# Kernel tuning notes

Measured on AMD Instinct MI355X. Metric: run time of the kernel, lower is better.

## Reference

```python
import jax, jax.numpy as jnp
import numpy as np

T, A = 2048, 64          # n_thread, n_agents
RAWOB, N_TP, N_GP = 120, 5, 2
E = N_TP * N_GP          # number of sub-nets (type x group placeholder)
D = RAWOB + N_TP + 1     # augmented obs dim fed to each Net
H = 128                  # hidden width of each sub-net MLP
N_ACTION = 16


def setup_inputs() -> dict:
    key = jax.random.key(0)
    ks = jax.random.split(key, 12)
    s1 = 1.0 / np.sqrt(D)
    s2 = 1.0 / np.sqrt(H)
    return {
        "obs": jax.random.normal(ks[0], (T, A, RAWOB), dtype=jnp.float32),
        "hete_pick": jax.random.randint(ks[1], (T, A), 0, E),
        "hete_type": jax.random.randint(ks[2], (T, A), 0, N_TP),
        "gp_sel_summary": jax.random.randint(ks[3], (T, N_TP), 0, N_GP),
        # per-expert actor MLP params [E, ...]
        "W1": jax.random.normal(ks[4], (E, D, H), dtype=jnp.float32) * s1,
        "b1": jnp.zeros((E, H), dtype=jnp.float32),
        "W2": jax.random.normal(ks[5], (E, H, N_ACTION), dtype=jnp.float32) * s2,
        "b2": jnp.zeros((E, N_ACTION), dtype=jnp.float32),
        # central critic params
        "Wc1": jax.random.normal(ks[6], (D, H), dtype=jnp.float32) * s1,
        "bc1": jnp.zeros((H,), dtype=jnp.float32),
        "Wc2": jax.random.normal(ks[7], (H, 1), dtype=jnp.float32) * s2,
        "bc2": jnp.zeros((1,), dtype=jnp.float32),
    }


def _augment_obs(obs, hete_type, gp_sel_summary):
    # obs <- cat(obs, hete_type, gp_sel_summary with -1 scattered at own type idx)
    t, a, _ = obs.shape
    n_tp = gp_sel_summary.shape[1]
    gp = jnp.broadcast_to(gp_sel_summary[:, None, :].astype(obs.dtype), (t, a, n_tp))
    oh = jax.nn.one_hot(hete_type, n_tp, dtype=obs.dtype)
    gp_obs = gp * (1.0 - oh) - oh  # scatter -1 at index hete_type
    return jnp.concatenate([obs, hete_type[..., None].astype(obs.dtype), gp_obs], axis=-1)


def reference(obs, hete_pick, hete_type, gp_sel_summary,
              W1, b1, W2, b2, Wc1, bc1, Wc2, bc2):
    t, a, _ = obs.shape
    x = _augment_obs(obs, hete_type, gp_sel_summary)          # [T, A, D]
    xf = x.reshape(t * a, -1)                                  # [N, D]
    pick = hete_pick.reshape(t * a)                            # [N]
    n_exp = W1.shape[0]
    # dispatch: each token routed to exactly one sub-net; dense compute + masked combine
    logits = jnp.zeros((t * a, W2.shape[-1]), dtype=obs.dtype)
    for e in range(n_exp):  # small fixed expert loop
        y = jax.nn.relu(xf @ W1[e] + b1[e]) @ W2[e] + b2[e]    # [N, n_action]
        logits = jnp.where((pick == e)[:, None], y, logits)
    logits = logits.reshape(t, a, -1)
    # central critic on all tokens
    value = (jax.nn.relu(xf @ Wc1 + bc1) @ Wc2 + bc2).reshape(t, a, 1)
    return logits, value
```

## Files before the change

kernel.cpp:

```cpp
#include <hip/hip_runtime.h>
#include <hip/hip_bf16.h>

#define T_DIM   2048
#define A_DIM   64
#define N_TOK   (T_DIM * A_DIM)
#define RAWOB   120
#define N_TP    5
#define E_EXP   10
#define D_DIM   126
#define DP      128
#define H_DIM   128
#define N_ACT   16
#define CAP     14336
#define MTILE   32
#define MAXC    (CAP / MTILE)
#define LOGITS_SZ (N_TOK * N_ACT)
#define XS_STRIDE 136

typedef __bf16 bh8 __attribute__((ext_vector_type(8)));
typedef float  f32x4 __attribute__((ext_vector_type(4)));

__device__ __forceinline__ f32x4 mfma16(bh8 a, bh8 b, f32x4 c) {
    return __builtin_amdgcn_mfma_f32_16x16x32_bf16(a, b, c, 0, 0, 0);
}

__device__ __forceinline__ ushort f2bf(float f) {
    unsigned x = __builtin_bit_cast(unsigned, f);
    unsigned r = (x + 0x7fffu + ((x >> 16) & 1u)) >> 16;
    return (ushort)r;
}

#define W1T_N (E_EXP * H_DIM * DP)
#define W2T_N (E_EXP * N_ACT * H_DIM)
#define WC1T_N (DP * DP)
#define PREP_BLOCKS 124

__global__ __launch_bounds__(256) void prep_kernel(
    const float* __restrict__ W1, const float* __restrict__ W2,
    const float* __restrict__ Wc1,
    int* __restrict__ counts, ushort* __restrict__ W1t,
    ushort* __restrict__ W2t, ushort* __restrict__ Wc1t)
{
    int bx = blockIdx.x, tid = threadIdx.x;
    if (bx < 44) {
        __shared__ ushort st[32][130];
        const float* src;
        ushort* dstbase;
        int d0;
        if (bx < 40) {
            int e = bx >> 2;
            d0 = (bx & 3) * 32;
            src = W1 + (e * D_DIM + d0) * H_DIM;
            dstbase = W1t + e * H_DIM * DP;
        } else {
            d0 = (bx - 40) * 32;
            src = Wc1 + d0 * H_DIM;
            dstbase = Wc1t;
        }
        int dmax = D_DIM - d0;
#pragma unroll
        for (int p = 0; p < 16; ++p) {
            int idx = p * 256 + tid;
            int dd = idx >> 7, h = idx & 127;
            float v = (dd < dmax) ? src[dd * H_DIM + h] : 0.f;
            st[dd][h] = f2bf(v);
        }
        __syncthreads();
#pragma unroll
        for (int p = 0; p < 16; ++p) {
            int idx = p * 256 + tid;
            int h = idx >> 5, d = idx & 31;
            dstbase[h * DP + d0 + d] = st[d][h];
        }
    } else {
        int i = (bx - 44) * 256 + tid;
        int h = i & 127;
        int a = (i >> 7) & 15;
        int e = i >> 11;
        W2t[(e * N_ACT + a) * H_DIM + h] = f2bf(W2[(e * H_DIM + h) * N_ACT + a]);
        if (bx == 44 && tid < 160) counts[tid] = 0;
    }
}

#define BUCKET_BLOCKS 128
__global__ __launch_bounds__(256) void bucket_kernel(
    const int* __restrict__ pick, int* __restrict__ counts, int* __restrict__ order)
{
    __shared__ int lc[E_EXP], lb[E_EXP], lcur[E_EXP];
    int tid = threadIdx.x;
    if (tid < E_EXP) { lc[tid] = 0; lcur[tid] = 0; }
    __syncthreads();
    int base = blockIdx.x * 1024;
    int e4[4];
#pragma unroll
    for (int it = 0; it < 4; ++it) {
        e4[it] = pick[base + it * 256 + tid];
        atomicAdd(&lc[e4[it]], 1);
    }
    __syncthreads();
    if (tid < E_EXP) lb[tid] = atomicAdd(&counts[tid * 16], lc[tid]);
    __syncthreads();
#pragma unroll
    for (int it = 0; it < 4; ++it) {
        int e = e4[it];
        int pos = lb[e] + atomicAdd(&lcur[e], 1);
        if (pos < CAP) order[e * CAP + pos] = base + it * 256 + tid;
    }
}

__global__ __launch_bounds__(256, 8) void moe_kernel(
    const float* __restrict__ obs, const int* __restrict__ hete_type,
    const int* __restrict__ gp_sel,
    const float* __restrict__ b1, const float* __restrict__ b2,
    const float* __restrict__ bc1, const float* __restrict__ bc2,
    const int* __restrict__ counts, const int* __restrict__ order,
    const ushort* __restrict__ W1t, const ushort* __restrict__ W2t,
    const ushort* __restrict__ Wc1t, const float* __restrict__ Wc2,
    float* __restrict__ out)
{
    __shared__ int idx_s[MTILE];
    __shared__ __align__(16) ushort xs[MTILE * XS_STRIDE];
    __shared__ __align__(16) ushort hs[MTILE * XS_STRIDE];
    __shared__ float red[4][MTILE];

    const int bx = blockIdx.x;
    const int e = bx % E_EXP;
    const int c = bx / E_EXP;
    const int cnt = counts[e * 16];
    const int start = c * MTILE;
    if (start >= cnt) return;
    const int v = min(MTILE, cnt - start);

    const int tid = threadIdx.x;
    if (tid < MTILE) {
        int tok = 0;
        if (tid < v) tok = order[e * CAP + start + tid];
        idx_s[tid] = tok;
    }
    __syncthreads();

    const int ck = (tid & 15) * 8;
    const int r0 = tid >> 4;
#pragma unroll
    for (int j = 0; j < 2; ++j) {
        int row = r0 + j * 16;
        int tok = idx_s[row];
        ushort* dst = &xs[row * XS_STRIDE + ck];
        if (ck < RAWOB) {
            const float* src = obs + tok * RAWOB + ck;
            float4 u0 = *(const float4*)(const void*)src;
            float4 u1 = *(const float4*)(const void*)(src + 4);
            dst[0] = f2bf(u0.x); dst[1] = f2bf(u0.y);
            dst[2] = f2bf(u0.z); dst[3] = f2bf(u0.w);
            dst[4] = f2bf(u1.x); dst[5] = f2bf(u1.y);
            dst[6] = f2bf(u1.z); dst[7] = f2bf(u1.w);
        } else {
            int ht = hete_type[tok];
            int tt = tok >> 6;
            dst[0] = f2bf((float)ht);
#pragma unroll
            for (int q = 0; q < N_TP; ++q) {
                float g = (q == ht) ? -1.0f : (float)gp_sel[tt * N_TP + q];
                dst[1 + q] = f2bf(g);
            }
            dst[6] = 0; dst[7] = 0;
        }
    }
    __syncthreads();

    const int w = tid >> 6;
    const int l = tid & 63;
    const int lm = l & 15;
    const int lq = l >> 4;
    const int n0 = w * 32;

    {
        const ushort* Wt = W1t + e * DP * DP;
        f32x4 acc[2][2];
#pragma unroll
        for (int mt = 0; mt < 2; ++mt) {
            acc[mt][0] = (f32x4){0.f, 0.f, 0.f, 0.f};
            acc[mt][1] = (f32x4){0.f, 0.f, 0.f, 0.f};
        }
#pragma unroll
        for (int kt = 0; kt < 4; ++kt) {
            bh8 bf0 = *(const bh8*)(const void*)(Wt + (n0 + lm) * DP + kt * 32 + lq * 8);
            bh8 bf1 = *(const bh8*)(const void*)(Wt + (n0 + 16 + lm) * DP + kt * 32 + lq * 8);
#pragma unroll
            for (int mt = 0; mt < 2; ++mt) {
                bh8 a = *(const bh8*)(const void*)
                    (xs + (mt * 16 + lm) * XS_STRIDE + kt * 32 + lq * 8);
                acc[mt][0] = mfma16(a, bf0, acc[mt][0]);
                acc[mt][1] = mfma16(a, bf1, acc[mt][1]);
            }
        }
        float bn0 = b1[e * H_DIM + n0 + lm];
        float bn1 = b1[e * H_DIM + n0 + 16 + lm];
#pragma unroll
        for (int mt = 0; mt < 2; ++mt)
#pragma unroll
            for (int nt = 0; nt < 2; ++nt) {
                float bn = nt ? bn1 : bn0;
                int n = n0 + nt * 16 + lm;
#pragma unroll
                for (int r = 0; r < 4; ++r) {
                    int m = mt * 16 + lq * 4 + r;
                    float vf = fmaxf(acc[mt][nt][r] + bn, 0.f);
                    hs[m * XS_STRIDE + n] = f2bf(vf);
                }
            }
    }
    __syncthreads();

    if (w < 2) {
        f32x4 acc2 = (f32x4){0.f, 0.f, 0.f, 0.f};
#pragma unroll
        for (int kt = 0; kt < 4; ++kt) {
            bh8 bf = *(const bh8*)(const void*)
                (W2t + (e * N_ACT + lm) * H_DIM + kt * 32 + lq * 8);
            bh8 a = *(const bh8*)(const void*)
                (hs + (w * 16 + lm) * XS_STRIDE + kt * 32 + lq * 8);
            acc2 = mfma16(a, bf, acc2);
        }
        float bb = b2[e * N_ACT + lm];
#pragma unroll
        for (int r = 0; r < 4; ++r) {
            int m = w * 16 + lq * 4 + r;
            if (m < v) {
                int tok = idx_s[m];
                out[tok * N_ACT + lm] = acc2[r] + bb;
            }
        }
    }

    {
        f32x4 acc[2][2];
#pragma unroll
        for (int mt = 0; mt < 2; ++mt) {
            acc[mt][0] = (f32x4){0.f, 0.f, 0.f, 0.f};
            acc[mt][1] = (f32x4){0.f, 0.f, 0.f, 0.f};
        }
#pragma unroll
        for (int kt = 0; kt < 4; ++kt) {
            bh8 bf0 = *(const bh8*)(const void*)(Wc1t + (n0 + lm) * DP + kt * 32 + lq * 8);
            bh8 bf1 = *(const bh8*)(const void*)(Wc1t + (n0 + 16 + lm) * DP + kt * 32 + lq * 8);
#pragma unroll
            for (int mt = 0; mt < 2; ++mt) {
                bh8 a = *(const bh8*)(const void*)
                    (xs + (mt * 16 + lm) * XS_STRIDE + kt * 32 + lq * 8);
                acc[mt][0] = mfma16(a, bf0, acc[mt][0]);
                acc[mt][1] = mfma16(a, bf1, acc[mt][1]);
            }
        }
        float bn0 = bc1[n0 + lm],   wcv0 = Wc2[n0 + lm];
        float bn1 = bc1[n0 + 16 + lm], wcv1 = Wc2[n0 + 16 + lm];
        float part[2][4];
#pragma unroll
        for (int mt = 0; mt < 2; ++mt)
#pragma unroll
            for (int r = 0; r < 4; ++r)
                part[mt][r] = fmaxf(acc[mt][0][r] + bn0, 0.f) * wcv0
                            + fmaxf(acc[mt][1][r] + bn1, 0.f) * wcv1;
#pragma unroll
        for (int mask = 1; mask < 16; mask <<= 1)
#pragma unroll
            for (int mt = 0; mt < 2; ++mt)
#pragma unroll
                for (int r = 0; r < 4; ++r)
                    part[mt][r] += __shfl_xor(part[mt][r], mask, 64);
        if (lm == 0) {
#pragma unroll
            for (int mt = 0; mt < 2; ++mt)
#pragma unroll
                for (int r = 0; r < 4; ++r)
                    red[w][mt * 16 + lq * 4 + r] = part[mt][r];
        }
    }
    __syncthreads();

    if (tid < MTILE && tid < v) {
        float vt = red[0][tid] + red[1][tid] + red[2][tid] + red[3][tid] + bc2[0];
        out[LOGITS_SZ + idx_s[tid]] = vt;
    }
}

extern "C" void kernel_launch(void* const* d_in, const int* in_sizes, int n_in,
                              void* d_out, int out_size, void* d_ws, size_t ws_size,
                              hipStream_t stream) {
    const float* obs  = (const float*)d_in[0];
    const int*   pick = (const int*)d_in[1];
    const int*   htyp = (const int*)d_in[2];
    const int*   gp   = (const int*)d_in[3];
    const float* W1   = (const float*)d_in[4];
    const float* b1   = (const float*)d_in[5];
    const float* W2   = (const float*)d_in[6];
    const float* b2   = (const float*)d_in[7];
    const float* Wc1  = (const float*)d_in[8];
    const float* bc1  = (const float*)d_in[9];
    const float* Wc2  = (const float*)d_in[10];
    const float* bc2  = (const float*)d_in[11];
    float* out = (float*)d_out;

    int*    counts = (int*)d_ws;
    int*    order  = counts + 160;
    ushort* W1t    = (ushort*)(order + E_EXP * CAP);
    ushort* W2t    = W1t + W1T_N;
    ushort* Wc1t   = W2t + W2T_N;

    prep_kernel<<<PREP_BLOCKS, 256, 0, stream>>>(
        W1, W2, Wc1, counts, W1t, W2t, Wc1t);
    bucket_kernel<<<BUCKET_BLOCKS, 256, 0, stream>>>(pick, counts, order);
    moe_kernel<<<E_EXP * MAXC, 256, 0, stream>>>(
        obs, htyp, gp, b1, b2, bc1, bc2, counts, order,
        W1t, W2t, Wc1t, Wc2, out);
}
```

Baseline: 160.5 us.

## Split critic into separate dense kernel and double expert tile rows

Moves the central critic MLP out of the gathered expert kernel into its own kernel that processes contiguous 64-token tiles without the bucket indirection. The expert kernel now handles 64 tokens per block (MTILE 64), and all four waves do the second GEMM. This is meant to cut the critic's gather overhead and the idle waves in layer 2. In exchange, obs is staged twice (once per kernel), adding a launch and extra global reads, and the expert kernel needs more registers at lower occupancy.

```diff
diff --git a/kernel.cpp b/kernel.cpp
--- a/kernel.cpp
+++ b/kernel.cpp
@@ -12,7 +12,7 @@
 #define H_DIM   128
 #define N_ACT   16
 #define CAP     14336
-#define MTILE   32
+#define MTILE   64
 #define MAXC    (CAP / MTILE)
 #define LOGITS_SZ (N_TOK * N_ACT)
 #define XS_STRIDE 136
@@ -108,20 +108,118 @@
     }
 }
 
-__global__ __launch_bounds__(256, 8) void moe_kernel(
+__device__ __forceinline__ void stage_row(
+    ushort* dst, const float* __restrict__ obs, const int* __restrict__ hete_type,
+    const int* __restrict__ gp_sel, int tok, int ck)
+{
+    if (ck < RAWOB) {
+        const float* src = obs + tok * RAWOB + ck;
+        float4 u0 = *(const float4*)(const void*)src;
+        float4 u1 = *(const float4*)(const void*)(src + 4);
+        dst[0] = f2bf(u0.x); dst[1] = f2bf(u0.y);
+        dst[2] = f2bf(u0.z); dst[3] = f2bf(u0.w);
+        dst[4] = f2bf(u1.x); dst[5] = f2bf(u1.y);
+        dst[6] = f2bf(u1.z); dst[7] = f2bf(u1.w);
+    } else {
+        int ht = hete_type[tok];
+        int tt = tok >> 6;
+        dst[0] = f2bf((float)ht);
+#pragma unroll
+        for (int q = 0; q < N_TP; ++q) {
+            float g = (q == ht) ? -1.0f : (float)gp_sel[tt * N_TP + q];
+            dst[1 + q] = f2bf(g);
+        }
+        dst[6] = 0; dst[7] = 0;
+    }
+}
+
+__global__ __launch_bounds__(256, 8) void critic_kernel(
+    const float* __restrict__ obs, const int* __restrict__ hete_type,
+    const int* __restrict__ gp_sel,
+    const float* __restrict__ bc1, const float* __restrict__ bc2,
+    const ushort* __restrict__ Wc1t, const float* __restrict__ Wc2,
+    float* __restrict__ out)
+{
+    __shared__ __align__(16) ushort xs[64 * XS_STRIDE];
+    __shared__ float red[4][64];
+
+    const int t0 = blockIdx.x * 64;
+    const int tid = threadIdx.x;
+    const int ck = (tid & 15) * 8;
+    const int r0 = tid >> 4;
+#pragma unroll
+    for (int j = 0; j < 4; ++j) {
+        int row = r0 + j * 16;
+        stage_row(&xs[row * XS_STRIDE + ck], obs, hete_type, gp_sel, t0 + row, ck);
+    }
+    __syncthreads();
+
+    const int w = tid >> 6;
+    const int l = tid & 63;
+    const int lm = l & 15;
+    const int lq = l >> 4;
+    const int n0 = w * 32;
+
+    f32x4 acc[4][2];
+#pragma unroll
+    for (int mt = 0; mt < 4; ++mt) {
+        acc[mt][0] = (f32x4){0.f, 0.f, 0.f, 0.f};
+        acc[mt][1] = (f32x4){0.f, 0.f, 0.f, 0.f};
+    }
+#pragma unroll
+    for (int kt = 0; kt < 4; ++kt) {
+        bh8 bf0 = *(const bh8*)(const void*)(Wc1t + (n0 + lm) * DP + kt * 32 + lq * 8);
+        bh8 bf1 = *(const bh8*)(const void*)(Wc1t + (n0 + 16 + lm) * DP + kt * 32 + lq * 8);
+#pragma unroll
+        for (int mt = 0; mt < 4; ++mt) {
+            bh8 a = *(const bh8*)(const void*)
+                (xs + (mt * 16 + lm) * XS_STRIDE + kt * 32 + lq * 8);
+            acc[mt][0] = mfma16(a, bf0, acc[mt][0]);
+            acc[mt][1] = mfma16(a, bf1, acc[mt][1]);
+        }
+    }
+    float bn0 = bc1[n0 + lm],      wcv0 = Wc2[n0 + lm];
+    float bn1 = bc1[n0 + 16 + lm], wcv1 = Wc2[n0 + 16 + lm];
+    float part[4][4];
+#pragma unroll
+    for (int mt = 0; mt < 4; ++mt)
+#pragma unroll
+        for (int r = 0; r < 4; ++r)
+            part[mt][r] = fmaxf(acc[mt][0][r] + bn0, 0.f) * wcv0
+                        + fmaxf(acc[mt][1][r] + bn1, 0.f) * wcv1;
+#pragma unroll
+    for (int mask = 1; mask < 16; mask <<= 1)
+#pragma unroll
+        for (int mt = 0; mt < 4; ++mt)
+#pragma unroll
+            for (int r = 0; r < 4; ++r)
+                part[mt][r] += __shfl_xor(part[mt][r], mask, 64);
+    if (lm == 0) {
+#pragma unroll
+        for (int mt = 0; mt < 4; ++mt)
+#pragma unroll
+            for (int r = 0; r < 4; ++r)
+                red[w][mt * 16 + lq * 4 + r] = part[mt][r];
+    }
+    __syncthreads();
+
+    if (tid < 64) {
+        out[LOGITS_SZ + t0 + tid] =
+            red[0][tid] + red[1][tid] + red[2][tid] + red[3][tid] + bc2[0];
+    }
+}
+
+__global__ __launch_bounds__(256, 4) void expert_kernel(
     const float* __restrict__ obs, const int* __restrict__ hete_type,
     const int* __restrict__ gp_sel,
     const float* __restrict__ b1, const float* __restrict__ b2,
-    const float* __restrict__ bc1, const float* __restrict__ bc2,
     const int* __restrict__ counts, const int* __restrict__ order,
     const ushort* __restrict__ W1t, const ushort* __restrict__ W2t,
-    const ushort* __restrict__ Wc1t, const float* __restrict__ Wc2,
     float* __restrict__ out)
 {
     __shared__ int idx_s[MTILE];
     __shared__ __align__(16) ushort xs[MTILE * XS_STRIDE];
     __shared__ __align__(16) ushort hs[MTILE * XS_STRIDE];
-    __shared__ float red[4][MTILE];
 
     const int bx = blockIdx.x;
     const int e = bx % E_EXP;
@@ -142,29 +240,9 @@
     const int ck = (tid & 15) * 8;
     const int r0 = tid >> 4;
 #pragma unroll
-    for (int j = 0; j < 2; ++j) {
+    for (int j = 0; j < 4; ++j) {
         int row = r0 + j * 16;
-        int tok = idx_s[row];
-        ushort* dst = &xs[row * XS_STRIDE + ck];
-        if (ck < RAWOB) {
-            const float* src = obs + tok * RAWOB + ck;
-            float4 u0 = *(const float4*)(const void*)src;
-            float4 u1 = *(const float4*)(const void*)(src + 4);
-            dst[0] = f2bf(u0.x); dst[1] = f2bf(u0.y);
-            dst[2] = f2bf(u0.z); dst[3] = f2bf(u0.w);
-            dst[4] = f2bf(u1.x); dst[5] = f2bf(u1.y);
-            dst[6] = f2bf(u1.z); dst[7] = f2bf(u1.w);
-        } else {
-            int ht = hete_type[tok];
-            int tt = tok >> 6;
-            dst[0] = f2bf((float)ht);
-#pragma unroll
-            for (int q = 0; q < N_TP; ++q) {
-                float g = (q == ht) ? -1.0f : (float)gp_sel[tt * N_TP + q];
-                dst[1 + q] = f2bf(g);
-            }
-            dst[6] = 0; dst[7] = 0;
-        }
+        stage_row(&xs[row * XS_STRIDE + ck], obs, hete_type, gp_sel, idx_s[row], ck);
     }
     __syncthreads();
 
@@ -176,9 +254,9 @@
 
     {
         const ushort* Wt = W1t + e * DP * DP;
-        f32x4 acc[2][2];
-#pragma unroll
-        for (int mt = 0; mt < 2; ++mt) {
+        f32x4 acc[4][2];
+#pragma unroll
+        for (int mt = 0; mt < 4; ++mt) {
             acc[mt][0] = (f32x4){0.f, 0.f, 0.f, 0.f};
             acc[mt][1] = (f32x4){0.f, 0.f, 0.f, 0.f};
         }
@@ -187,7 +265,7 @@
             bh8 bf0 = *(const bh8*)(const void*)(Wt + (n0 + lm) * DP + kt * 32 + lq * 8);
             bh8 bf1 = *(const bh8*)(const void*)(Wt + (n0 + 16 + lm) * DP + kt * 32 + lq * 8);
 #pragma unroll
-            for (int mt = 0; mt < 2; ++mt) {
+            for (int mt = 0; mt < 4; ++mt) {
                 bh8 a = *(const bh8*)(const void*)
                     (xs + (mt * 16 + lm) * XS_STRIDE + kt * 32 + lq * 8);
                 acc[mt][0] = mfma16(a, bf0, acc[mt][0]);
@@ -197,7 +275,7 @@
         float bn0 = b1[e * H_DIM + n0 + lm];
         float bn1 = b1[e * H_DIM + n0 + 16 + lm];
 #pragma unroll
-        for (int mt = 0; mt < 2; ++mt)
+        for (int mt = 0; mt < 4; ++mt)
 #pragma unroll
             for (int nt = 0; nt < 2; ++nt) {
                 float bn = nt ? bn1 : bn0;
@@ -212,7 +290,7 @@
     }
     __syncthreads();
 
-    if (w < 2) {
+    {
         f32x4 acc2 = (f32x4){0.f, 0.f, 0.f, 0.f};
 #pragma unroll
         for (int kt = 0; kt < 4; ++kt) {
@@ -231,56 +309,6 @@
                 out[tok * N_ACT + lm] = acc2[r] + bb;
             }
         }
-    }
-
-    {
-        f32x4 acc[2][2];
-#pragma unroll
-        for (int mt = 0; mt < 2; ++mt) {
-            acc[mt][0] = (f32x4){0.f, 0.f, 0.f, 0.f};
-            acc[mt][1] = (f32x4){0.f, 0.f, 0.f, 0.f};
-        }
-#pragma unroll
-        for (int kt = 0; kt < 4; ++kt) {
-            bh8 bf0 = *(const bh8*)(const void*)(Wc1t + (n0 + lm) * DP + kt * 32 + lq * 8);
-            bh8 bf1 = *(const bh8*)(const void*)(Wc1t + (n0 + 16 + lm) * DP + kt * 32 + lq * 8);
-#pragma unroll
-            for (int mt = 0; mt < 2; ++mt) {
-                bh8 a = *(const bh8*)(const void*)
-                    (xs + (mt * 16 + lm) * XS_STRIDE + kt * 32 + lq * 8);
-                acc[mt][0] = mfma16(a, bf0, acc[mt][0]);
-                acc[mt][1] = mfma16(a, bf1, acc[mt][1]);
-            }
-        }
-        float bn0 = bc1[n0 + lm],   wcv0 = Wc2[n0 + lm];
-        float bn1 = bc1[n0 + 16 + lm], wcv1 = Wc2[n0 + 16 + lm];
-        float part[2][4];
-#pragma unroll
-        for (int mt = 0; mt < 2; ++mt)
-#pragma unroll
-            for (int r = 0; r < 4; ++r)
-                part[mt][r] = fmaxf(acc[mt][0][r] + bn0, 0.f) * wcv0
-                            + fmaxf(acc[mt][1][r] + bn1, 0.f) * wcv1;
-#pragma unroll
-        for (int mask = 1; mask < 16; mask <<= 1)
-#pragma unroll
-            for (int mt = 0; mt < 2; ++mt)
-#pragma unroll
-                for (int r = 0; r < 4; ++r)
-                    part[mt][r] += __shfl_xor(part[mt][r], mask, 64);
-        if (lm == 0) {
-#pragma unroll
-            for (int mt = 0; mt < 2; ++mt)
-#pragma unroll
-                for (int r = 0; r < 4; ++r)
-                    red[w][mt * 16 + lq * 4 + r] = part[mt][r];
-        }
-    }
-    __syncthreads();
-
-    if (tid < MTILE && tid < v) {
-        float vt = red[0][tid] + red[1][tid] + red[2][tid] + red[3][tid] + bc2[0];
-        out[LOGITS_SZ + idx_s[tid]] = vt;
     }
 }
 
@@ -310,7 +338,8 @@
     prep_kernel<<<PREP_BLOCKS, 256, 0, stream>>>(
         W1, W2, Wc1, counts, W1t, W2t, Wc1t);
     bucket_kernel<<<BUCKET_BLOCKS, 256, 0, stream>>>(pick, counts, order);
-    moe_kernel<<<E_EXP * MAXC, 256, 0, stream>>>(
-        obs, htyp, gp, b1, b2, bc1, bc2, counts, order,
-        W1t, W2t, Wc1t, Wc2, out);
-}
+    critic_kernel<<<N_TOK / 64, 256, 0, stream>>>(
+        obs, htyp, gp, bc1, bc2, Wc1t, Wc2, out);
+    expert_kernel<<<E_EXP * MAXC, 256, 0, stream>>>(
+        obs, htyp, gp, b1, b2, counts, order, W1t, W2t, out);
+}
```

Result: slower. 173.1 us (+7.9%).

## Double token tile to 64 and reuse one LDS buffer for hidden activations

Applied to the files above, without the earlier changes.

Doubles the per-block token tile from 32 to 64 rows, so each block reuses the loaded W1/Wc1 fragments across four M-subtiles and half as many blocks are launched. The critic GEMM now runs first, before the hidden activations overwrite the input tile in the same shared buffer. That drops the separate hs buffer and keeps LDS usage roughly flat. All four waves now do the second expert GEMM instead of two, at the cost of more accumulator registers per thread, which may lower occupancy, and fewer blocks to spread across CUs.

```diff
diff --git a/kernel.cpp b/kernel.cpp
--- a/kernel.cpp
+++ b/kernel.cpp
@@ -12,7 +12,7 @@
 #define H_DIM   128
 #define N_ACT   16
 #define CAP     14336
-#define MTILE   32
+#define MTILE   64
 #define MAXC    (CAP / MTILE)
 #define LOGITS_SZ (N_TOK * N_ACT)
 #define XS_STRIDE 136
@@ -108,6 +108,31 @@
     }
 }
 
+__device__ __forceinline__ void stage_row(
+    ushort* dst, const float* __restrict__ obs, const int* __restrict__ hete_type,
+    const int* __restrict__ gp_sel, int tok, int ck)
+{
+    if (ck < RAWOB) {
+        const float* src = obs + tok * RAWOB + ck;
+        float4 u0 = *(const float4*)(const void*)src;
+        float4 u1 = *(const float4*)(const void*)(src + 4);
+        dst[0] = f2bf(u0.x); dst[1] = f2bf(u0.y);
+        dst[2] = f2bf(u0.z); dst[3] = f2bf(u0.w);
+        dst[4] = f2bf(u1.x); dst[5] = f2bf(u1.y);
+        dst[6] = f2bf(u1.z); dst[7] = f2bf(u1.w);
+    } else {
+        int ht = hete_type[tok];
+        int tt = tok >> 6;
+        dst[0] = f2bf((float)ht);
+#pragma unroll
+        for (int q = 0; q < N_TP; ++q) {
+            float g = (q == ht) ? -1.0f : (float)gp_sel[tt * N_TP + q];
+            dst[1 + q] = f2bf(g);
+        }
+        dst[6] = 0; dst[7] = 0;
+    }
+}
+
 __global__ __launch_bounds__(256, 8) void moe_kernel(
     const float* __restrict__ obs, const int* __restrict__ hete_type,
     const int* __restrict__ gp_sel,
@@ -120,7 +145,6 @@
 {
     __shared__ int idx_s[MTILE];
     __shared__ __align__(16) ushort xs[MTILE * XS_STRIDE];
-    __shared__ __align__(16) ushort hs[MTILE * XS_STRIDE];
     __shared__ float red[4][MTILE];
 
     const int bx = blockIdx.x;
@@ -142,29 +166,9 @@
     const int ck = (tid & 15) * 8;
     const int r0 = tid >> 4;
 #pragma unroll
-    for (int j = 0; j < 2; ++j) {
+    for (int j = 0; j < 4; ++j) {
         int row = r0 + j * 16;
-        int tok = idx_s[row];
-        ushort* dst = &xs[row * XS_STRIDE + ck];
-        if (ck < RAWOB) {
-            const float* src = obs + tok * RAWOB + ck;
-            float4 u0 = *(const float4*)(const void*)src;
-            float4 u1 = *(const float4*)(const void*)(src + 4);
-            dst[0] = f2bf(u0.x); dst[1] = f2bf(u0.y);
-            dst[2] = f2bf(u0.z); dst[3] = f2bf(u0.w);
-            dst[4] = f2bf(u1.x); dst[5] = f2bf(u1.y);
-            dst[6] = f2bf(u1.z); dst[7] = f2bf(u1.w);
-        } else {
-            int ht = hete_type[tok];
-            int tt = tok >> 6;
-            dst[0] = f2bf((float)ht);
-#pragma unroll
-            for (int q = 0; q < N_TP; ++q) {
-                float g = (q == ht) ? -1.0f : (float)gp_sel[tt * N_TP + q];
-                dst[1 + q] = f2bf(g);
-            }
-            dst[6] = 0; dst[7] = 0;
-        }
+        stage_row(&xs[row * XS_STRIDE + ck], obs, hete_type, gp_sel, idx_s[row], ck);
     }
     __syncthreads();
 
@@ -175,29 +179,78 @@
     const int n0 = w * 32;
 
     {
+        float part[4][4];
+#pragma unroll
+        for (int mt = 0; mt < 4; ++mt)
+#pragma unroll
+            for (int r = 0; r < 4; ++r) part[mt][r] = 0.f;
+#pragma unroll
+        for (int nt = 0; nt < 2; ++nt) {
+            int n = n0 + nt * 16 + lm;
+            f32x4 acc[4];
+#pragma unroll
+            for (int mt = 0; mt < 4; ++mt) acc[mt] = (f32x4){0.f, 0.f, 0.f, 0.f};
+#pragma unroll
+            for (int kt = 0; kt < 4; ++kt) {
+                bh8 bf = *(const bh8*)(const void*)(Wc1t + n * DP + kt * 32 + lq * 8);
+#pragma unroll
+                for (int mt = 0; mt < 4; ++mt) {
+                    bh8 a = *(const bh8*)(const void*)
+                        (xs + (mt * 16 + lm) * XS_STRIDE + kt * 32 + lq * 8);
+                    acc[mt] = mfma16(a, bf, acc[mt]);
+                }
+            }
+            float bn = bc1[n], wcv = Wc2[n];
+#pragma unroll
+            for (int mt = 0; mt < 4; ++mt)
+#pragma unroll
+                for (int r = 0; r < 4; ++r)
+                    part[mt][r] += fmaxf(acc[mt][r] + bn, 0.f) * wcv;
+        }
+#pragma unroll
+        for (int mask = 1; mask < 16; mask <<= 1)
+#pragma unroll
+            for (int mt = 0; mt < 4; ++mt)
+#pragma unroll
+                for (int r = 0; r < 4; ++r)
+                    part[mt][r] += __shfl_xor(part[mt][r], mask, 64);
+        if (lm == 0) {
+#pragma unroll
+            for (int mt = 0; mt < 4; ++mt)
+#pragma unroll
+                for (int r = 0; r < 4; ++r)
+                    red[w][mt * 16 + lq * 4 + r] = part[mt][r];
+        }
+    }
+
+    f32x4 acc[4][2];
+#pragma unroll
+    for (int mt = 0; mt < 4; ++mt) {
+        acc[mt][0] = (f32x4){0.f, 0.f, 0.f, 0.f};
+        acc[mt][1] = (f32x4){0.f, 0.f, 0.f, 0.f};
+    }
+    {
         const ushort* Wt = W1t + e * DP * DP;
-        f32x4 acc[2][2];
-#pragma unroll
-        for (int mt = 0; mt < 2; ++mt) {
-            acc[mt][0] = (f32x4){0.f, 0.f, 0.f, 0.f};
-            acc[mt][1] = (f32x4){0.f, 0.f, 0.f, 0.f};
-        }
 #pragma unroll
         for (int kt = 0; kt < 4; ++kt) {
             bh8 bf0 = *(const bh8*)(const void*)(Wt + (n0 + lm) * DP + kt * 32 + lq * 8);
             bh8 bf1 = *(const bh8*)(const void*)(Wt + (n0 + 16 + lm) * DP + kt * 32 + lq * 8);
 #pragma unroll
-            for (int mt = 0; mt < 2; ++mt) {
+            for (int mt = 0; mt < 4; ++mt) {
                 bh8 a = *(const bh8*)(const void*)
                     (xs + (mt * 16 + lm) * XS_STRIDE + kt * 32 + lq * 8);
                 acc[mt][0] = mfma16(a, bf0, acc[mt][0]);
                 acc[mt][1] = mfma16(a, bf1, acc[mt][1]);
             }
         }
+    }
+    __syncthreads();
+
+    {
         float bn0 = b1[e * H_DIM + n0 + lm];
         float bn1 = b1[e * H_DIM + n0 + 16 + lm];
 #pragma unroll
-        for (int mt = 0; mt < 2; ++mt)
+        for (int mt = 0; mt < 4; ++mt)
 #pragma unroll
             for (int nt = 0; nt < 2; ++nt) {
                 float bn = nt ? bn1 : bn0;
@@ -206,20 +259,20 @@
                 for (int r = 0; r < 4; ++r) {
                     int m = mt * 16 + lq * 4 + r;
                     float vf = fmaxf(acc[mt][nt][r] + bn, 0.f);
-                    hs[m * XS_STRIDE + n] = f2bf(vf);
+                    xs[m * XS_STRIDE + n] = f2bf(vf);
                 }
             }
     }
     __syncthreads();
 
-    if (w < 2) {
+    {
         f32x4 acc2 = (f32x4){0.f, 0.f, 0.f, 0.f};
 #pragma unroll
         for (int kt = 0; kt < 4; ++kt) {
             bh8 bf = *(const bh8*)(const void*)
                 (W2t + (e * N_ACT + lm) * H_DIM + kt * 32 + lq * 8);
             bh8 a = *(const bh8*)(const void*)
-                (hs + (w * 16 + lm) * XS_STRIDE + kt * 32 + lq * 8);
+                (xs + (w * 16 + lm) * XS_STRIDE + kt * 32 + lq * 8);
             acc2 = mfma16(a, bf, acc2);
         }
         float bb = b2[e * N_ACT + lm];
@@ -232,51 +285,6 @@
             }
         }
     }
-
-    {
-        f32x4 acc[2][2];
-#pragma unroll
-        for (int mt = 0; mt < 2; ++mt) {
-            acc[mt][0] = (f32x4){0.f, 0.f, 0.f, 0.f};
-            acc[mt][1] = (f32x4){0.f, 0.f, 0.f, 0.f};
-        }
-#pragma unroll
-        for (int kt = 0; kt < 4; ++kt) {
-            bh8 bf0 = *(const bh8*)(const void*)(Wc1t + (n0 + lm) * DP + kt * 32 + lq * 8);
-            bh8 bf1 = *(const bh8*)(const void*)(Wc1t + (n0 + 16 + lm) * DP + kt * 32 + lq * 8);
-#pragma unroll
-            for (int mt = 0; mt < 2; ++mt) {
-                bh8 a = *(const bh8*)(const void*)
-                    (xs + (mt * 16 + lm) * XS_STRIDE + kt * 32 + lq * 8);
-                acc[mt][0] = mfma16(a, bf0, acc[mt][0]);
-                acc[mt][1] = mfma16(a, bf1, acc[mt][1]);
-            }
-        }
-        float bn0 = bc1[n0 + lm],   wcv0 = Wc2[n0 + lm];
-        float bn1 = bc1[n0 + 16 + lm], wcv1 = Wc2[n0 + 16 + lm];
-        float part[2][4];
-#pragma unroll
-        for (int mt = 0; mt < 2; ++mt)
-#pragma unroll
-            for (int r = 0; r < 4; ++r)
-                part[mt][r] = fmaxf(acc[mt][0][r] + bn0, 0.f) * wcv0
-                            + fmaxf(acc[mt][1][r] + bn1, 0.f) * wcv1;
-#pragma unroll
-        for (int mask = 1; mask < 16; mask <<= 1)
-#pragma unroll
-            for (int mt = 0; mt < 2; ++mt)
-#pragma unroll
-                for (int r = 0; r < 4; ++r)
-                    part[mt][r] += __shfl_xor(part[mt][r], mask, 64);
-        if (lm == 0) {
-#pragma unroll
-            for (int mt = 0; mt < 2; ++mt)
-#pragma unroll
-                for (int r = 0; r < 4; ++r)
-                    red[w][mt * 16 + lq * 4 + r] = part[mt][r];
-        }
-    }
-    __syncthreads();
 
     if (tid < MTILE && tid < v) {
         float vt = red[0][tid] + red[1][tid] + red[2][tid] + red[3][tid] + bc2[0];
```

Measured after the change: 164.9 us. 1.03x slower.
